# Kernel tuning notes

Hardware: AMD Instinct MI355X
Metric: run time of the kernel (lower is better)

## Reference

```python
import jax, jax.numpy as jnp
import numpy as np

S, B, C = 7, 2, 20
N = B * 5 + C  # 30
L_COORD, L_NOOBJ = 5.0, 0.5


def setup_inputs() -> dict:
    key = jax.random.key(0)
    k1, k2, k3, k4 = jax.random.split(key, 4)
    batch = 16384
    pred = jax.random.uniform(k1, (batch, S, S, N), dtype=jnp.float32)
    target = jax.random.uniform(k2, (batch, S, S, N), dtype=jnp.float32)
    # rescale w/h channels of both boxes to [0.5, 1) so the (buggy) in-place
    # coordinate transform never yields negative values under sqrt
    wh_idx = jnp.array([2, 3, 7, 8])
    pred = pred.at[..., wh_idx].set(0.5 + 0.5 * pred[..., wh_idx])
    target = target.at[..., wh_idx].set(0.5 + 0.5 * target[..., wh_idx])
    obj = jax.random.uniform(k3, (batch, S, S)) < 0.25
    conf = 0.1 + 0.9 * jax.random.uniform(k4, (batch, S, S))
    target = target.at[..., 4].set(jnp.where(obj, conf, 0.0))
    return {"pred": pred, "target": target}


def _yolo_loss(pred, target):
    # Faithful vectorization of the original loop-y torch forward, bugs included:
    #  * x2y2 is computed from the ALREADY transformed xy (xy_new/S + 0.5*wh)
    #  * lambda_coord only multiplies the x / sqrt(w) terms, not y / sqrt(h)
    #  * the selected per-cell loss SUMS l1+l2+l3+IoU (IoU itself is added)
    #  * only the first min(S^2, #coord_cells) coord cells (global flatten
    #    order across the batch) contribute to bbox_loss
    #  * class-prob loss slices dim1 of a [M,2,5] tensor with 10: -> empty -> 0
    p = pred.reshape(-1, N)   # [M, 30], M = b*S*S, row-major like torch mask gather
    t = target.reshape(-1, N)
    obj = t[:, 4] > 0
    rank = jnp.cumsum(obj.astype(jnp.int32)) - 1  # rank among coord cells
    active = obj & (rank < S * S)                 # cells whose bbox loss counts

    pb = p[:, :10].reshape(-1, B, 5)  # [M, B, 5]
    tb = t[:, :10].reshape(-1, B, 5)

    def transform(box):
        xy = box[..., :2] / S - 0.5 * box[..., 2:4]      # new x1,y1
        x2y2 = xy / S + 0.5 * box[..., 2:4]              # uses NEW xy (original bug)
        return xy, x2y2

    pxy, p2 = transform(pb)
    txy, t2 = transform(tb)

    l1 = L_COORD * (txy[..., 0] - pxy[..., 0]) ** 2 + (txy[..., 1] - pxy[..., 1]) ** 2
    l2 = (L_COORD * (jnp.sqrt(t2[..., 0]) - jnp.sqrt(p2[..., 0])) ** 2
          + (jnp.sqrt(t2[..., 1]) - jnp.sqrt(p2[..., 1])) ** 2)
    l3 = (tb[..., 4] - pb[..., 4]) ** 2

    # IoU between pred box j and target box j (boxes as [x1,y1,x2,y2])
    lt = jnp.maximum(pxy, txy)
    rb = jnp.minimum(p2, t2)
    wh = jnp.maximum(rb - lt, 0.0)
    inter = wh[..., 0] * wh[..., 1]
    area_p = (p2[..., 0] - pxy[..., 0]) * (p2[..., 1] - pxy[..., 1])
    area_t = (t2[..., 0] - txy[..., 0]) * (t2[..., 1] - txy[..., 1])
    iou = inter / (area_p + area_t - inter)  # [M, B]

    tot = l1 + l2 + l3 + iou                 # sum(info[argmax]) includes IoU
    jstar = jnp.argmax(iou, axis=1)          # responsible box per cell
    sel = jnp.take_along_axis(tot, jstar[:, None], axis=1)[:, 0]
    bbox_loss = jnp.sum(jnp.where(active, sel, 0.0))

    # no-object confidence loss over both boxes' conf channels (4 and 9)
    noobj = ~obj
    conf_sq = (p[:, 4] - t[:, 4]) ** 2 + (p[:, 9] - t[:, 9]) ** 2
    noobj_loss = L_NOOBJ * jnp.sum(jnp.where(noobj, conf_sq, 0.0))

    # class prob loss: original slices [:, 10:] on a [M, B, 5] tensor -> empty -> 0
    class_prob_loss = jnp.float32(0.0)

    return bbox_loss + noobj_loss + class_prob_loss


def reference(pred, target):
    return _yolo_loss(pred, target)
```

## Files before the change

### kernel.cpp

```cpp
#include <hip/hip_runtime.h>

#define NCH 30
#define RANK_LIMIT 49
#define L_COORD 5.0f
#define L_NOOBJ 0.5f

#define NB 5880
#define UNROLL 4

typedef float vfloat4 __attribute__((ext_vector_type(4)));

__global__ __launch_bounds__(256) void noobj_kernel(const vfloat4* __restrict__ pv,
                                                    const vfloat4* __restrict__ tv,
                                                    const float* __restrict__ ts,
                                                    float* __restrict__ partials) {
    const int tid  = threadIdx.x;
    const int lane = tid & 63;
    const int base = blockIdx.x * (256 * UNROLL) + tid;

    vfloat4 vp[UNROLL], vt[UNROLL];
    #pragma unroll
    for (int u = 0; u < UNROLL; ++u) {
        int i = base + u * 256;
        vp[u] = __builtin_nontemporal_load(&pv[i]);
        vt[u] = __builtin_nontemporal_load(&tv[i]);
    }

    float acc = 0.0f;
    #pragma unroll
    for (int u = 0; u < UNROLL; ++u) {
        int i = base + u * 256;
        int pair = i / 15;
        int k = i - pair * 15;

        float gx = __shfl_up(vt[u].x, 1, 64);
        float gz = __shfl_up(vt[u].z, 1, 64);
        if (lane == 0) {
            if (k == 2) gx = ts[pair * 60 + 4];
            if (k == 9) gz = ts[pair * 60 + 34];
        }

        float d1 = vp[u].x - vt[u].x;
        float d2 = vp[u].y - vt[u].y;
        float d8 = vp[u].z - vt[u].z;
        float d9 = vp[u].w - vt[u].w;

        float c1 = (!(vt[u].x > 0.0f)) ? d1 * d1 : 0.0f;
        float c2 = (!(gx      > 0.0f)) ? d2 * d2 : 0.0f;
        float c8 = (!(vt[u].z > 0.0f)) ? d8 * d8 : 0.0f;
        float c9 = (!(gz      > 0.0f)) ? d9 * d9 : 0.0f;

        float contrib = (k == 1) ? c1 : (k == 2) ? c2 : (k == 8) ? c8
                      : (k == 9) ? c9 : 0.0f;
        acc += contrib;
    }

    #pragma unroll
    for (int off = 32; off > 0; off >>= 1)
        acc += __shfl_down(acc, off, 64);
    __shared__ float s[4];
    int wid = tid >> 6;
    if (lane == 0) s[wid] = acc;
    __syncthreads();
    if (tid == 0)
        partials[blockIdx.x] = s[0] + s[1] + s[2] + s[3];
}

__device__ inline float sel_loss(const float* __restrict__ p,
                                 const float* __restrict__ t, int row) {
    const float invS = 1.0f / 7.0f;
    int b0 = row * NCH;
    float tot0 = 0.f, tot1 = 0.f, iou0 = 0.f, iou1 = 0.f;
    #pragma unroll
    for (int j = 0; j < 2; ++j) {
        int o = b0 + 5 * j;
        float px = p[o + 0], py = p[o + 1], pw = p[o + 2], ph = p[o + 3], pc = p[o + 4];
        float tx = t[o + 0], ty = t[o + 1], tw = t[o + 2], th = t[o + 3], tc = t[o + 4];
        float pxy0 = px * invS - 0.5f * pw;
        float pxy1 = py * invS - 0.5f * ph;
        float p2x  = pxy0 * invS + 0.5f * pw;
        float p2y  = pxy1 * invS + 0.5f * ph;
        float txy0 = tx * invS - 0.5f * tw;
        float txy1 = ty * invS - 0.5f * th;
        float t2x  = txy0 * invS + 0.5f * tw;
        float t2y  = txy1 * invS + 0.5f * th;
        float d0 = txy0 - pxy0, d1 = txy1 - pxy1;
        float l1 = L_COORD * d0 * d0 + d1 * d1;
        float s0 = sqrtf(t2x) - sqrtf(p2x);
        float s1 = sqrtf(t2y) - sqrtf(p2y);
        float l2 = L_COORD * s0 * s0 + s1 * s1;
        float dc = tc - pc;
        float l3 = dc * dc;
        float ltx = fmaxf(pxy0, txy0), lty = fmaxf(pxy1, txy1);
        float rbx = fminf(p2x, t2x),   rby = fminf(p2y, t2y);
        float wx  = fmaxf(rbx - ltx, 0.0f);
        float wy  = fmaxf(rby - lty, 0.0f);
        float inter  = wx * wy;
        float area_p = (p2x - pxy0) * (p2y - pxy1);
        float area_t = (t2x - txy0) * (t2y - txy1);
        float io = inter / (area_p + area_t - inter);
        float tt = l1 + l2 + l3 + io;
        if (j == 0) { iou0 = io; tot0 = tt; }
        else        { iou1 = io; tot1 = tt; }
    }
    return (iou1 > iou0) ? tot1 : tot0;
}

__global__ __launch_bounds__(256) void bbox_kernel(const float* __restrict__ p,
                                                   const float* __restrict__ t,
                                                   const float* __restrict__ partials,
                                                   float* __restrict__ out, int M) {
    __shared__ int   s_wcnt[4];
    __shared__ int   s_base;
    __shared__ float s_part[4];
    if (threadIdx.x == 0) s_base = 0;
    __syncthreads();

    float local = 0.0f;
    for (int start = 0; start < M; start += 256) {
        int row = start + (int)threadIdx.x;
        bool obj = false;
        if (row < M) obj = t[row * NCH + 4] > 0.0f;

        unsigned long long mask = __ballot(obj);
        int lane = threadIdx.x & 63;
        int wid  = threadIdx.x >> 6;
        if (lane == 0) s_wcnt[wid] = __popcll(mask);
        __syncthreads();

        int base = s_base;
        int off = 0;
        for (int w = 0; w < wid; ++w) off += s_wcnt[w];
        int rank = base + off + __popcll(mask & ((1ULL << lane) - 1ULL));
        if (obj && rank < RANK_LIMIT) local += sel_loss(p, t, row);
        __syncthreads();

        if (threadIdx.x == 0)
            s_base = base + s_wcnt[0] + s_wcnt[1] + s_wcnt[2] + s_wcnt[3];
        __syncthreads();
        if (s_base >= RANK_LIMIT) break;
    }

    for (int i = threadIdx.x; i < NB; i += 256)
        local += L_NOOBJ * partials[i];

    #pragma unroll
    for (int o = 32; o > 0; o >>= 1)
        local += __shfl_down(local, o, 64);
    int lane = threadIdx.x & 63;
    int wid  = threadIdx.x >> 6;
    if (lane == 0) s_part[wid] = local;
    __syncthreads();
    if (threadIdx.x == 0)
        out[0] = s_part[0] + s_part[1] + s_part[2] + s_part[3];
}

extern "C" void kernel_launch(void* const* d_in, const int* in_sizes, int n_in,
                              void* d_out, int out_size, void* d_ws, size_t ws_size,
                              hipStream_t stream) {
    const float* pred = (const float*)d_in[0];
    const float* targ = (const float*)d_in[1];
    float* out = (float*)d_out;
    float* partials = (float*)d_ws;

    int M = in_sizes[0] / NCH;

    noobj_kernel<<<NB, 256, 0, stream>>>((const vfloat4*)pred, (const vfloat4*)targ,
                                         targ, partials);
    bbox_kernel<<<1, 256, 0, stream>>>(pred, targ, partials, out, M);
}
```

Measured before the change: 197.0 us.

## Fuse noobj and bbox kernels into one launch with atomic last-block reduction

```diff
diff --git a/kernel.cpp b/kernel.cpp
--- a/kernel.cpp
+++ b/kernel.cpp
@@ -5,65 +5,34 @@
 #define L_COORD 5.0f
 #define L_NOOBJ 0.5f
 
-#define NB 5880
-#define UNROLL 4
+#define NB 2940
+#define UNROLL 8
+#define NBLK_TOTAL (NB + 1)
 
 typedef float vfloat4 __attribute__((ext_vector_type(4)));
 
-__global__ __launch_bounds__(256) void noobj_kernel(const vfloat4* __restrict__ pv,
-                                                    const vfloat4* __restrict__ tv,
-                                                    const float* __restrict__ ts,
-                                                    float* __restrict__ partials) {
-    const int tid  = threadIdx.x;
-    const int lane = tid & 63;
-    const int base = blockIdx.x * (256 * UNROLL) + tid;
-
-    vfloat4 vp[UNROLL], vt[UNROLL];
-    #pragma unroll
-    for (int u = 0; u < UNROLL; ++u) {
-        int i = base + u * 256;
-        vp[u] = __builtin_nontemporal_load(&pv[i]);
-        vt[u] = __builtin_nontemporal_load(&tv[i]);
-    }
-
-    float acc = 0.0f;
-    #pragma unroll
-    for (int u = 0; u < UNROLL; ++u) {
-        int i = base + u * 256;
-        int pair = i / 15;
-        int k = i - pair * 15;
-
-        float gx = __shfl_up(vt[u].x, 1, 64);
-        float gz = __shfl_up(vt[u].z, 1, 64);
-        if (lane == 0) {
-            if (k == 2) gx = ts[pair * 60 + 4];
-            if (k == 9) gz = ts[pair * 60 + 34];
-        }
-
-        float d1 = vp[u].x - vt[u].x;
-        float d2 = vp[u].y - vt[u].y;
-        float d8 = vp[u].z - vt[u].z;
-        float d9 = vp[u].w - vt[u].w;
-
-        float c1 = (!(vt[u].x > 0.0f)) ? d1 * d1 : 0.0f;
-        float c2 = (!(gx      > 0.0f)) ? d2 * d2 : 0.0f;
-        float c8 = (!(vt[u].z > 0.0f)) ? d8 * d8 : 0.0f;
-        float c9 = (!(gz      > 0.0f)) ? d9 * d9 : 0.0f;
-
-        float contrib = (k == 1) ? c1 : (k == 2) ? c2 : (k == 8) ? c8
-                      : (k == 9) ? c9 : 0.0f;
-        acc += contrib;
-    }
-
+__device__ inline float block_reduce(float v) {
     #pragma unroll
     for (int off = 32; off > 0; off >>= 1)
-        acc += __shfl_down(acc, off, 64);
+        v += __shfl_down(v, off, 64);
     __shared__ float s[4];
-    int wid = tid >> 6;
-    if (lane == 0) s[wid] = acc;
+    int lane = threadIdx.x & 63, wid = threadIdx.x >> 6;
+    if (lane == 0) s[wid] = v;
     __syncthreads();
-    if (tid == 0)
-        partials[blockIdx.x] = s[0] + s[1] + s[2] + s[3];
+    return (threadIdx.x == 0) ? (s[0] + s[1] + s[2] + s[3]) : 0.0f;
+}
+
+__device__ inline void finish_block(float contrib, float* acc, int* cnt,
+                                    float* out) {
+    if (threadIdx.x == 0) {
+        atomicAdd(acc, contrib);
+        __threadfence();
+        int old = atomicAdd(cnt, 1);
+        if (old == NBLK_TOTAL - 1) {
+            float tot = atomicAdd(acc, 0.0f);
+            out[0] = tot;
+        }
+    }
 }
 
 __device__ inline float sel_loss(const float* __restrict__ p,
@@ -106,53 +75,89 @@
     return (iou1 > iou0) ? tot1 : tot0;
 }
 
-__global__ __launch_bounds__(256) void bbox_kernel(const float* __restrict__ p,
-                                                   const float* __restrict__ t,
-                                                   const float* __restrict__ partials,
+__global__ __launch_bounds__(256) void yolo_kernel(const vfloat4* __restrict__ pv,
+                                                   const vfloat4* __restrict__ tv,
+                                                   const float* __restrict__ ps,
+                                                   const float* __restrict__ ts,
+                                                   float* __restrict__ acc,
+                                                   int* __restrict__ cnt,
                                                    float* __restrict__ out, int M) {
-    __shared__ int   s_wcnt[4];
-    __shared__ int   s_base;
-    __shared__ float s_part[4];
-    if (threadIdx.x == 0) s_base = 0;
-    __syncthreads();
+    const int tid  = threadIdx.x;
+    const int lane = tid & 63;
 
-    float local = 0.0f;
-    for (int start = 0; start < M; start += 256) {
-        int row = start + (int)threadIdx.x;
-        bool obj = false;
-        if (row < M) obj = t[row * NCH + 4] > 0.0f;
+    if (blockIdx.x < NB) {
+        const int base = blockIdx.x * (256 * UNROLL) + tid;
+        vfloat4 vp[UNROLL], vt[UNROLL];
+        #pragma unroll
+        for (int u = 0; u < UNROLL; ++u) {
+            int i = base + u * 256;
+            vp[u] = __builtin_nontemporal_load(&pv[i]);
+            vt[u] = __builtin_nontemporal_load(&tv[i]);
+        }
 
-        unsigned long long mask = __ballot(obj);
-        int lane = threadIdx.x & 63;
-        int wid  = threadIdx.x >> 6;
-        if (lane == 0) s_wcnt[wid] = __popcll(mask);
+        float s_acc = 0.0f;
+        #pragma unroll
+        for (int u = 0; u < UNROLL; ++u) {
+            int i = base + u * 256;
+            int pair = i / 15;
+            int k = i - pair * 15;
+
+            float gx = __shfl_up(vt[u].x, 1, 64);
+            float gz = __shfl_up(vt[u].z, 1, 64);
+            if (lane == 0) {
+                if (k == 2) gx = ts[pair * 60 + 4];
+                if (k == 9) gz = ts[pair * 60 + 34];
+            }
+
+            float d1 = vp[u].x - vt[u].x;
+            float d2 = vp[u].y - vt[u].y;
+            float d8 = vp[u].z - vt[u].z;
+            float d9 = vp[u].w - vt[u].w;
+
+            float c1 = (!(vt[u].x > 0.0f)) ? d1 * d1 : 0.0f;
+            float c2 = (!(gx      > 0.0f)) ? d2 * d2 : 0.0f;
+            float c8 = (!(vt[u].z > 0.0f)) ? d8 * d8 : 0.0f;
+            float c9 = (!(gz      > 0.0f)) ? d9 * d9 : 0.0f;
+
+            s_acc += (k == 1) ? c1 : (k == 2) ? c2 : (k == 8) ? c8
+                   : (k == 9) ? c9 : 0.0f;
+        }
+
+        float part = block_reduce(s_acc);
+        finish_block(L_NOOBJ * part, acc, cnt, out);
+    } else {
+        __shared__ int s_wcnt[4];
+        __shared__ int s_base;
+        if (tid == 0) s_base = 0;
         __syncthreads();
 
-        int base = s_base;
-        int off = 0;
-        for (int w = 0; w < wid; ++w) off += s_wcnt[w];
-        int rank = base + off + __popcll(mask & ((1ULL << lane) - 1ULL));
-        if (obj && rank < RANK_LIMIT) local += sel_loss(p, t, row);
-        __syncthreads();
+        float local = 0.0f;
+        for (int start = 0; start < M; start += 256) {
+            int row = start + tid;
+            bool obj = false;
+            if (row < M) obj = ts[row * NCH + 4] > 0.0f;
 
-        if (threadIdx.x == 0)
-            s_base = base + s_wcnt[0] + s_wcnt[1] + s_wcnt[2] + s_wcnt[3];
-        __syncthreads();
-        if (s_base >= RANK_LIMIT) break;
+            unsigned long long mask = __ballot(obj);
+            int wid = tid >> 6;
+            if (lane == 0) s_wcnt[wid] = __popcll(mask);
+            __syncthreads();
+
+            int base = s_base;
+            int off = 0;
+            for (int w = 0; w < wid; ++w) off += s_wcnt[w];
+            int rank = base + off + __popcll(mask & ((1ULL << lane) - 1ULL));
+            if (obj && rank < RANK_LIMIT) local += sel_loss(ps, ts, row);
+            __syncthreads();
+
+            if (tid == 0)
+                s_base = base + s_wcnt[0] + s_wcnt[1] + s_wcnt[2] + s_wcnt[3];
+            __syncthreads();
+            if (s_base >= RANK_LIMIT) break;
+        }
+
+        float part = block_reduce(local);
+        finish_block(part, acc, cnt, out);
     }
-
-    for (int i = threadIdx.x; i < NB; i += 256)
-        local += L_NOOBJ * partials[i];
-
-    #pragma unroll
-    for (int o = 32; o > 0; o >>= 1)
-        local += __shfl_down(local, o, 64);
-    int lane = threadIdx.x & 63;
-    int wid  = threadIdx.x >> 6;
-    if (lane == 0) s_part[wid] = local;
-    __syncthreads();
-    if (threadIdx.x == 0)
-        out[0] = s_part[0] + s_part[1] + s_part[2] + s_part[3];
 }
 
 extern "C" void kernel_launch(void* const* d_in, const int* in_sizes, int n_in,
@@ -161,11 +166,13 @@
     const float* pred = (const float*)d_in[0];
     const float* targ = (const float*)d_in[1];
     float* out = (float*)d_out;
-    float* partials = (float*)d_ws;
+    float* acc = (float*)d_ws;
+    int*   cnt = (int*)d_ws + 1;
 
     int M = in_sizes[0] / NCH;
 
-    noobj_kernel<<<NB, 256, 0, stream>>>((const vfloat4*)pred, (const vfloat4*)targ,
-                                         targ, partials);
-    bbox_kernel<<<1, 256, 0, stream>>>(pred, targ, partials, out, M);
+    hipMemsetAsync(d_ws, 0, 8, stream);
+
+    yolo_kernel<<<NBLK_TOTAL, 256, 0, stream>>>(
+        (const vfloat4*)pred, (const vfloat4*)targ, pred, targ, acc, cnt, out, M);
 }
```

Result: slower. 327.7 us (+66.3%).
